# Performance work log

Measured on AMD Instinct MI355X. Metric: run time of the kernel, lower is better.

## Reference

```python
import jax, jax.numpy as jnp
import numpy as np
from jax import lax

B = 512
MBD_B, MBD_C = 64, 16
FEAT = 40 * 4 * 4  # 640


def _conv(x, w, b):
    y = lax.conv_general_dilated(x, w, (1, 1), 'VALID',
                                 dimension_numbers=('NCHW', 'OIHW', 'NCHW'))
    return y + b[None, :, None, None]


def _maxpool2(x):
    return lax.reduce_window(x, -jnp.inf, lax.max,
                             (1, 1, 2, 2), (1, 1, 2, 2), 'VALID')


def setup_inputs() -> dict:
    key = jax.random.key(0)
    ks = jax.random.split(key, 10)
    def he(k, shape, fan_in):
        return jax.random.normal(k, shape, dtype=jnp.float32) * np.float32(1.0 / np.sqrt(fan_in))
    return {
        'x': jax.random.normal(ks[0], (B, 1, 28, 28), dtype=jnp.float32),
        'conv1_w': he(ks[1], (20, 1, 5, 5), 25),
        'conv1_b': jnp.zeros((20,), jnp.float32),
        'conv2_w': he(ks[2], (40, 20, 5, 5), 20 * 25),
        'conv2_b': jnp.zeros((40,), jnp.float32),
        'T': he(ks[3], (MBD_B * MBD_C, FEAT), FEAT),          # feature_scan_tensor (no bias)
        'fc1_w': he(ks[4], (100, FEAT + MBD_B), FEAT + MBD_B),
        'fc1_b': jnp.zeros((100,), jnp.float32),
        'fc2_w': he(ks[5], (1, 100), 100),
        'fc2_b': jnp.zeros((1,), jnp.float32),
    }


def reference(x, conv1_w, conv1_b, conv2_w, conv2_b, T, fc1_w, fc1_b, fc2_w, fc2_b):
    # conv feature extractor: [B,1,28,28] -> [B,40,4,4]
    h = _maxpool2(jax.nn.relu(_conv(x, conv1_w, conv1_b)))
    h = _maxpool2(jax.nn.relu(_conv(h, conv2_w, conv2_b)))
    feats = h.reshape(h.shape[0], -1)  # [B, 640]

    # minibatch discrimination: M = feats @ T^T -> [B, b, c]
    M = (feats @ T.T).reshape(-1, MBD_B, MBD_C)
    # pairwise L1 over c: [B, B, b] (includes j==i diagonal = 0, exp(0)=1, as in original)
    dist = jnp.abs(M[:, None, :, :] - M[None, :, :, :]).sum(axis=3)
    closeness = jnp.exp(-dist).sum(axis=1)  # [B, b]

    out = jnp.concatenate([feats, closeness], axis=1)  # [B, 640+b]
    out = jax.nn.relu(out @ fc1_w.T + fc1_b)
    # Dropout(p=0.2) omitted (deterministic eval-mode reference)
    out = jax.nn.sigmoid(out @ fc2_w.T + fc2_b)  # [B, 1]
    return out
```

## Files before the change

### kernel.cpp

```cpp
#include <hip/hip_runtime.h>


#define NB 512

__global__ __launch_bounds__(256) void k1_conv1_pool(
    const float* __restrict__ x, const float* __restrict__ w,
    const float* __restrict__ bias, float* __restrict__ out) {
  __shared__ float img[784];
  __shared__ float wl[500];
  __shared__ float bl[20];
  const int imgId = blockIdx.x;
  {
    const float4* src = reinterpret_cast<const float4*>(x + imgId * 784);
    float4* dst = reinterpret_cast<float4*>(img);
    for (int t = threadIdx.x; t < 196; t += 256) dst[t] = src[t];
  }
  for (int t = threadIdx.x; t < 500; t += 256) wl[t] = w[t];
  if (threadIdx.x < 20) bl[threadIdx.x] = bias[threadIdx.x];
  __syncthreads();

  for (int o = threadIdx.x; o < 2880; o += 256) {
    const int ch = o / 144;
    const int rem = o - ch * 144;
    const int py = rem / 12;
    const int px = rem - py * 12;
    const int oy = py * 2, ox = px * 2;
    float p[6][6];
    const float* ib = &img[oy * 28 + ox];
#pragma unroll
    for (int r = 0; r < 6; ++r) {
      const float2 v0 = *reinterpret_cast<const float2*>(&ib[r * 28 + 0]);
      const float2 v1 = *reinterpret_cast<const float2*>(&ib[r * 28 + 2]);
      const float2 v2 = *reinterpret_cast<const float2*>(&ib[r * 28 + 4]);
      p[r][0] = v0.x; p[r][1] = v0.y; p[r][2] = v1.x;
      p[r][3] = v1.y; p[r][4] = v2.x; p[r][5] = v2.y;
    }
    const float* wc = &wl[ch * 25];
    float s00 = 0.f, s01 = 0.f, s10 = 0.f, s11 = 0.f;
#pragma unroll
    for (int ky = 0; ky < 5; ++ky) {
#pragma unroll
      for (int kx = 0; kx < 5; ++kx) {
        const float ww = wc[ky * 5 + kx];
        s00 += p[ky][kx] * ww;
        s01 += p[ky][kx + 1] * ww;
        s10 += p[ky + 1][kx] * ww;
        s11 += p[ky + 1][kx + 1] * ww;
      }
    }
    const float m = fmaxf(fmaxf(s00, s01), fmaxf(s10, s11)) + bl[ch];
    out[imgId * 2880 + o] = fmaxf(m, 0.f);
  }
}

__global__ __launch_bounds__(256) void k2_conv2_pool(
    const float* __restrict__ h1, const float* __restrict__ w,
    const float* __restrict__ bias, float* __restrict__ feats) {
  __shared__ float in[2880];
  __shared__ float wt[2][2][25][64];
  __shared__ float part[128][21];
  const int imgId = blockIdx.x;
  const int tid = threadIdx.x;
  const int h = tid >> 7;
  const int chg = (tid >> 4) & 7;
  const int pos = tid & 15;
  const int py = pos >> 2, px = pos & 3;
  const int oy = py * 2, ox = px * 2;

  {
    const float4* src = reinterpret_cast<const float4*>(h1 + imgId * 2880);
    float4* dst = reinterpret_cast<float4*>(in);
    for (int t = tid; t < 720; t += 256) dst[t] = src[t];
  }
  for (int e = tid; e < 2000; e += 256) {
    const int eh = (e >= 1000) ? 1 : 0;
    const int e2 = e - eh * 1000;
    const int oc = e2 / 25, tap = e2 - oc * 25;
    wt[eh][0][tap][(oc / 5) * 8 + (oc - (oc / 5) * 5)] =
        w[oc * 500 + (eh ? 10 : 0) * 25 + tap];
  }
  __syncthreads();

  float acc[5][4];
#pragma unroll
  for (int q = 0; q < 5; ++q)
#pragma unroll
    for (int pp = 0; pp < 4; ++pp) acc[q][pp] = 0.f;

  for (int s = 0; s < 10; ++s) {
    const int p0 = s & 1;
    float sv[8];
    if (s < 9) {
#pragma unroll
      for (int k = 0; k < 8; ++k) {
        const int e = tid + k * 256;
        if (e < 2000) {
          const int eh = (e >= 1000) ? 1 : 0;
          const int e2 = e - eh * 1000;
          const int oc = e2 / 25, tap = e2 - oc * 25;
          const int ic = eh ? (11 + s) : (s + 1);
          sv[k] = w[oc * 500 + ic * 25 + tap];
        }
      }
    }
    const int myic = h * 10 + s;
    float p[6][6];
    {
      const float* ib = &in[myic * 144 + oy * 12 + ox];
#pragma unroll
      for (int r = 0; r < 6; ++r) {
        const float2 v0 = *reinterpret_cast<const float2*>(&ib[r * 12 + 0]);
        const float2 v1 = *reinterpret_cast<const float2*>(&ib[r * 12 + 2]);
        const float2 v2 = *reinterpret_cast<const float2*>(&ib[r * 12 + 4]);
        p[r][0] = v0.x; p[r][1] = v0.y; p[r][2] = v1.x;
        p[r][3] = v1.y; p[r][4] = v2.x; p[r][5] = v2.y;
      }
    }
#pragma unroll
    for (int ky = 0; ky < 5; ++ky) {
#pragma unroll
      for (int kx = 0; kx < 5; ++kx) {
        const int tap = ky * 5 + kx;
        const float4 w4 =
            *reinterpret_cast<const float4*>(&wt[h][p0][tap][chg * 8]);
        const float w4b = wt[h][p0][tap][chg * 8 + 4];
        const float i00 = p[ky][kx];
        const float i01 = p[ky][kx + 1];
        const float i10 = p[ky + 1][kx];
        const float i11 = p[ky + 1][kx + 1];
        acc[0][0] += i00 * w4.x; acc[0][1] += i01 * w4.x;
        acc[0][2] += i10 * w4.x; acc[0][3] += i11 * w4.x;
        acc[1][0] += i00 * w4.y; acc[1][1] += i01 * w4.y;
        acc[1][2] += i10 * w4.y; acc[1][3] += i11 * w4.y;
        acc[2][0] += i00 * w4.z; acc[2][1] += i01 * w4.z;
        acc[2][2] += i10 * w4.z; acc[2][3] += i11 * w4.z;
        acc[3][0] += i00 * w4.w; acc[3][1] += i01 * w4.w;
        acc[3][2] += i10 * w4.w; acc[3][3] += i11 * w4.w;
        acc[4][0] += i00 * w4b; acc[4][1] += i01 * w4b;
        acc[4][2] += i10 * w4b; acc[4][3] += i11 * w4b;
      }
    }
    if (s < 9) {
#pragma unroll
      for (int k = 0; k < 8; ++k) {
        const int e = tid + k * 256;
        if (e < 2000) {
          const int eh = (e >= 1000) ? 1 : 0;
          const int e2 = e - eh * 1000;
          const int oc = e2 / 25, tap = e2 - oc * 25;
          wt[eh][(s + 1) & 1][tap][(oc / 5) * 8 + (oc - (oc / 5) * 5)] = sv[k];
        }
      }
    }
    __syncthreads();
  }

  if (tid >= 128) {
    const int t2 = tid - 128;
#pragma unroll
    for (int q = 0; q < 5; ++q)
#pragma unroll
      for (int pp = 0; pp < 4; ++pp) part[t2][q * 4 + pp] = acc[q][pp];
  }
  __syncthreads();
  if (tid < 128) {
#pragma unroll
    for (int q = 0; q < 5; ++q) {
      const int ch = chg * 5 + q;
      const float a0 = acc[q][0] + part[tid][q * 4 + 0];
      const float a1 = acc[q][1] + part[tid][q * 4 + 1];
      const float a2 = acc[q][2] + part[tid][q * 4 + 2];
      const float a3 = acc[q][3] + part[tid][q * 4 + 3];
      const float m = fmaxf(fmaxf(a0, a1), fmaxf(a2, a3)) + bias[ch];
      feats[imgId * 640 + ch * 16 + pos] = fmaxf(m, 0.f);
    }
  }
}

__global__ __launch_bounds__(256) void k3_gemm(
    const float* __restrict__ A, const float* __restrict__ Bm,
    float* __restrict__ C) {
  __shared__ float As[16][68];
  __shared__ float Bs[16][36];
  const int tid = threadIdx.x;
  const int tx = tid & 15;
  const int ty = tid >> 4;
  const int i0 = blockIdx.y * 64;
  const int j0 = blockIdx.x * 32;
  float acc[4][2];
#pragma unroll
  for (int u = 0; u < 4; ++u)
#pragma unroll
    for (int v = 0; v < 2; ++v) acc[u][v] = 0.f;

  for (int k0 = 0; k0 < 640; k0 += 16) {
    {
      const int m = tid >> 2, kq = tid & 3;
      const float4 av =
          *reinterpret_cast<const float4*>(A + (i0 + m) * 640 + k0 + kq * 4);
      As[kq * 4 + 0][m] = av.x;
      As[kq * 4 + 1][m] = av.y;
      As[kq * 4 + 2][m] = av.z;
      As[kq * 4 + 3][m] = av.w;
    }
    if (tid < 128) {
      const int n = tid >> 2, kq = tid & 3;
      const float4 bv =
          *reinterpret_cast<const float4*>(Bm + (j0 + n) * 640 + k0 + kq * 4);
      Bs[kq * 4 + 0][n] = bv.x;
      Bs[kq * 4 + 1][n] = bv.y;
      Bs[kq * 4 + 2][n] = bv.z;
      Bs[kq * 4 + 3][n] = bv.w;
    }
    __syncthreads();
#pragma unroll
    for (int kk = 0; kk < 16; ++kk) {
      const float4 a4 = *reinterpret_cast<const float4*>(&As[kk][ty * 4]);
      const float2 b2 = *reinterpret_cast<const float2*>(&Bs[kk][tx * 2]);
      acc[0][0] += a4.x * b2.x; acc[0][1] += a4.x * b2.y;
      acc[1][0] += a4.y * b2.x; acc[1][1] += a4.y * b2.y;
      acc[2][0] += a4.z * b2.x; acc[2][1] += a4.z * b2.y;
      acc[3][0] += a4.w * b2.x; acc[3][1] += a4.w * b2.y;
    }
    __syncthreads();
  }
#pragma unroll
  for (int u = 0; u < 4; ++u) {
    float2 st = make_float2(acc[u][0], acc[u][1]);
    *reinterpret_cast<float2*>(&C[(i0 + ty * 4 + u) * 1024 + j0 + tx * 2]) = st;
  }
}

__global__ __launch_bounds__(256) void k4_mbd(const float* __restrict__ M,
                                              float* __restrict__ cp) {
  const int bid = blockIdx.x;
  const int ig = bid >> 4;
  const int jq = bid & 15;
  const int t = threadIdx.x;
  const int b = t & 63;
  const int g = t >> 6;
  const int i0 = ig * 16 + g * 4;
  float4 mi[4][4];
#pragma unroll
  for (int u = 0; u < 4; ++u) {
    const float4* mp = reinterpret_cast<const float4*>(M + (i0 + u) * 1024 + b * 16);
    mi[u][0] = mp[0]; mi[u][1] = mp[1]; mi[u][2] = mp[2]; mi[u][3] = mp[3];
  }
  float acc[4] = {0.f, 0.f, 0.f, 0.f};
  for (int jj = 0; jj < 32; ++jj) {
    const int j = jq * 32 + jj;
    const float4* mjp = reinterpret_cast<const float4*>(M + j * 1024 + b * 16);
    const float4 mj0 = mjp[0], mj1 = mjp[1], mj2 = mjp[2], mj3 = mjp[3];
#pragma unroll
    for (int u = 0; u < 4; ++u) {
      float dist =
          fabsf(mi[u][0].x - mj0.x) + fabsf(mi[u][0].y - mj0.y) +
          fabsf(mi[u][0].z - mj0.z) + fabsf(mi[u][0].w - mj0.w) +
          fabsf(mi[u][1].x - mj1.x) + fabsf(mi[u][1].y - mj1.y) +
          fabsf(mi[u][1].z - mj1.z) + fabsf(mi[u][1].w - mj1.w) +
          fabsf(mi[u][2].x - mj2.x) + fabsf(mi[u][2].y - mj2.y) +
          fabsf(mi[u][2].z - mj2.z) + fabsf(mi[u][2].w - mj2.w) +
          fabsf(mi[u][3].x - mj3.x) + fabsf(mi[u][3].y - mj3.y) +
          fabsf(mi[u][3].z - mj3.z) + fabsf(mi[u][3].w - mj3.w);
      acc[u] += __expf(-dist);
    }
  }
#pragma unroll
  for (int u = 0; u < 4; ++u)
    cp[(jq * 512 + i0 + u) * 64 + b] = acc[u];
}

__global__ __launch_bounds__(128) void k5_head(
    const float* __restrict__ feats, const float* __restrict__ cp,
    const float* __restrict__ w1, const float* __restrict__ b1,
    const float* __restrict__ w2, const float* __restrict__ b2,
    float* __restrict__ out) {
  __shared__ float v[704];
  __shared__ float hb[100];
  const int i = blockIdx.x;
  for (int t = threadIdx.x; t < 640; t += 128) v[t] = feats[i * 640 + t];
  if (threadIdx.x < 64) {
    float s = 0.f;
#pragma unroll
    for (int q = 0; q < 16; ++q) s += cp[(q * 512 + i) * 64 + threadIdx.x];
    v[640 + threadIdx.x] = s;
  }
  __syncthreads();
  const int k = threadIdx.x;
  if (k < 100) {
    const float* wr = w1 + k * 704;
    float s = b1[k];
#pragma unroll 4
    for (int d = 0; d < 704; d += 4) {
      const float4 wv = *reinterpret_cast<const float4*>(wr + d);
      s += v[d] * wv.x + v[d + 1] * wv.y + v[d + 2] * wv.z + v[d + 3] * wv.w;
    }
    hb[k] = fmaxf(s, 0.f) * w2[k];
  }
  __syncthreads();
  if (threadIdx.x == 0) {
    float s = b2[0];
#pragma unroll 4
    for (int q = 0; q < 100; ++q) s += hb[q];
    out[i] = 1.f / (1.f + __expf(-s));
  }
}

extern "C" void kernel_launch(void* const* d_in, const int* in_sizes, int n_in,
                              void* d_out, int out_size, void* d_ws,
                              size_t ws_size, hipStream_t stream) {
  const float* x   = (const float*)d_in[0];
  const float* c1w = (const float*)d_in[1];
  const float* c1b = (const float*)d_in[2];
  const float* c2w = (const float*)d_in[3];
  const float* c2b = (const float*)d_in[4];
  const float* T   = (const float*)d_in[5];
  const float* f1w = (const float*)d_in[6];
  const float* f1b = (const float*)d_in[7];
  const float* f2w = (const float*)d_in[8];
  const float* f2b = (const float*)d_in[9];
  float* out = (float*)d_out;

  float* h1    = (float*)d_ws;
  float* feats = h1 + 512 * 2880;
  float* M     = feats + 512 * 640;
  float* cp    = h1;

  k1_conv1_pool<<<NB, 256, 0, stream>>>(x, c1w, c1b, h1);
  k2_conv2_pool<<<NB, 256, 0, stream>>>(h1, c2w, c2b, feats);
  k3_gemm<<<dim3(32, 8), 256, 0, stream>>>(feats, T, M);
  k4_mbd<<<NB, 256, 0, stream>>>(M, cp);
  k5_head<<<NB, 128, 0, stream>>>(feats, cp, f1w, f1b, f2w, f2b, out);
}
```

Measured before the change: 203.8 us.

## Split conv kernels per channel half, pre-transform conv2 weights, stage MBD rows in LDS

```diff
diff --git a/kernel.cpp b/kernel.cpp
--- a/kernel.cpp
+++ b/kernel.cpp
@@ -1,27 +1,43 @@
 #include <hip/hip_runtime.h>
 
 
-#define NB 512
-
-__global__ __launch_bounds__(256) void k1_conv1_pool(
+__global__ __launch_bounds__(256) void k0_wxform(const float* __restrict__ w,
+                                                 float* __restrict__ ws) {
+  const int e = blockIdx.x * 256 + threadIdx.x;
+  if (e >= 32000) return;
+  const int ocHalf = e / 16000;
+  const int r = e - ocHalf * 16000;
+  const int ic = r / 800;
+  const int r2 = r - ic * 800;
+  const int tap = r2 >> 5;
+  const int slot = r2 & 31;
+  const int q = slot & 7;
+  const int grp = slot >> 3;
+  float val = 0.f;
+  if (q < 5) val = w[(ocHalf * 20 + grp * 5 + q) * 500 + ic * 25 + tap];
+  ws[e] = val;
+}
+
+__global__ __launch_bounds__(128) void k1_conv1_pool(
     const float* __restrict__ x, const float* __restrict__ w,
     const float* __restrict__ bias, float* __restrict__ out) {
-  __shared__ float img[784];
-  __shared__ float wl[500];
-  __shared__ float bl[20];
-  const int imgId = blockIdx.x;
+  __shared__ __align__(16) float img[784];
+  __shared__ float wl[250];
+  __shared__ float bl[10];
+  const int imgId = blockIdx.x >> 1;
+  const int half = blockIdx.x & 1;
   {
     const float4* src = reinterpret_cast<const float4*>(x + imgId * 784);
     float4* dst = reinterpret_cast<float4*>(img);
-    for (int t = threadIdx.x; t < 196; t += 256) dst[t] = src[t];
-  }
-  for (int t = threadIdx.x; t < 500; t += 256) wl[t] = w[t];
-  if (threadIdx.x < 20) bl[threadIdx.x] = bias[threadIdx.x];
-  __syncthreads();
-
-  for (int o = threadIdx.x; o < 2880; o += 256) {
-    const int ch = o / 144;
-    const int rem = o - ch * 144;
+    for (int t = threadIdx.x; t < 196; t += 128) dst[t] = src[t];
+  }
+  for (int t = threadIdx.x; t < 250; t += 128) wl[t] = w[half * 250 + t];
+  if (threadIdx.x < 10) bl[threadIdx.x] = bias[half * 10 + threadIdx.x];
+  __syncthreads();
+
+  for (int o = threadIdx.x; o < 1440; o += 128) {
+    const int chl = o / 144;
+    const int rem = o - chl * 144;
     const int py = rem / 12;
     const int px = rem - py * 12;
     const int oy = py * 2, ox = px * 2;
@@ -35,7 +51,7 @@
       p[r][0] = v0.x; p[r][1] = v0.y; p[r][2] = v1.x;
       p[r][3] = v1.y; p[r][4] = v2.x; p[r][5] = v2.y;
     }
-    const float* wc = &wl[ch * 25];
+    const float* wc = &wl[chl * 25];
     float s00 = 0.f, s01 = 0.f, s10 = 0.f, s11 = 0.f;
 #pragma unroll
     for (int ky = 0; ky < 5; ++ky) {
@@ -48,21 +64,22 @@
         s11 += p[ky + 1][kx + 1] * ww;
       }
     }
-    const float m = fmaxf(fmaxf(s00, s01), fmaxf(s10, s11)) + bl[ch];
-    out[imgId * 2880 + o] = fmaxf(m, 0.f);
-  }
-}
-
-__global__ __launch_bounds__(256) void k2_conv2_pool(
-    const float* __restrict__ h1, const float* __restrict__ w,
+    const float m = fmaxf(fmaxf(s00, s01), fmaxf(s10, s11)) + bl[chl];
+    out[imgId * 2880 + half * 1440 + o] = fmaxf(m, 0.f);
+  }
+}
+
+__global__ __launch_bounds__(128) void k2_conv2_pool(
+    const float* __restrict__ h1, const float* __restrict__ wsx,
     const float* __restrict__ bias, float* __restrict__ feats) {
-  __shared__ float in[2880];
-  __shared__ float wt[2][2][25][64];
-  __shared__ float part[128][21];
-  const int imgId = blockIdx.x;
+  __shared__ __align__(16) float in[2880];
+  __shared__ __align__(16) float wl[2][2][25][32];
+  __shared__ float part[64][21];
+  const int imgId = blockIdx.x >> 1;
+  const int half = blockIdx.x & 1;
   const int tid = threadIdx.x;
-  const int h = tid >> 7;
-  const int chg = (tid >> 4) & 7;
+  const int h = tid >> 6;
+  const int grp = (tid >> 4) & 3;
   const int pos = tid & 15;
   const int py = pos >> 2, px = pos & 3;
   const int oy = py * 2, ox = px * 2;
@@ -70,14 +87,20 @@
   {
     const float4* src = reinterpret_cast<const float4*>(h1 + imgId * 2880);
     float4* dst = reinterpret_cast<float4*>(in);
-    for (int t = tid; t < 720; t += 256) dst[t] = src[t];
-  }
-  for (int e = tid; e < 2000; e += 256) {
-    const int eh = (e >= 1000) ? 1 : 0;
-    const int e2 = e - eh * 1000;
-    const int oc = e2 / 25, tap = e2 - oc * 25;
-    wt[eh][0][tap][(oc / 5) * 8 + (oc - (oc / 5) * 5)] =
-        w[oc * 500 + (eh ? 10 : 0) * 25 + tap];
+    for (int t = tid; t < 720; t += 128) dst[t] = src[t];
+  }
+  const float4* wsrc = reinterpret_cast<const float4*>(wsx) + half * 4000;
+  float4* wdst = reinterpret_cast<float4*>(wl);
+  {
+#pragma unroll
+    for (int k = 0; k < 4; ++k) {
+      const int e = tid + k * 128;
+      if (e < 400) {
+        const int hs = (e >= 200) ? 1 : 0;
+        const int idx = e - hs * 200;
+        wdst[hs * 400 + idx] = wsrc[(hs * 10 + 0) * 200 + idx];
+      }
+    }
   }
   __syncthreads();
 
@@ -89,17 +112,15 @@
 
   for (int s = 0; s < 10; ++s) {
     const int p0 = s & 1;
-    float sv[8];
+    float4 sv[4];
     if (s < 9) {
 #pragma unroll
-      for (int k = 0; k < 8; ++k) {
-        const int e = tid + k * 256;
-        if (e < 2000) {
-          const int eh = (e >= 1000) ? 1 : 0;
-          const int e2 = e - eh * 1000;
-          const int oc = e2 / 25, tap = e2 - oc * 25;
-          const int ic = eh ? (11 + s) : (s + 1);
-          sv[k] = w[oc * 500 + ic * 25 + tap];
+      for (int k = 0; k < 4; ++k) {
+        const int e = tid + k * 128;
+        if (e < 400) {
+          const int hs = (e >= 200) ? 1 : 0;
+          const int idx = e - hs * 200;
+          sv[k] = wsrc[(hs * 10 + s + 1) * 200 + idx];
         }
       }
     }
@@ -122,8 +143,8 @@
       for (int kx = 0; kx < 5; ++kx) {
         const int tap = ky * 5 + kx;
         const float4 w4 =
-            *reinterpret_cast<const float4*>(&wt[h][p0][tap][chg * 8]);
-        const float w4b = wt[h][p0][tap][chg * 8 + 4];
+            *reinterpret_cast<const float4*>(&wl[h][p0][tap][grp * 8]);
+        const float w4b = wl[h][p0][tap][grp * 8 + 4];
         const float i00 = p[ky][kx];
         const float i01 = p[ky][kx + 1];
         const float i10 = p[ky + 1][kx];
@@ -142,31 +163,30 @@
     }
     if (s < 9) {
 #pragma unroll
-      for (int k = 0; k < 8; ++k) {
-        const int e = tid + k * 256;
-        if (e < 2000) {
-          const int eh = (e >= 1000) ? 1 : 0;
-          const int e2 = e - eh * 1000;
-          const int oc = e2 / 25, tap = e2 - oc * 25;
-          wt[eh][(s + 1) & 1][tap][(oc / 5) * 8 + (oc - (oc / 5) * 5)] = sv[k];
+      for (int k = 0; k < 4; ++k) {
+        const int e = tid + k * 128;
+        if (e < 400) {
+          const int hs = (e >= 200) ? 1 : 0;
+          const int idx = e - hs * 200;
+          wdst[hs * 400 + ((s + 1) & 1) * 200 + idx] = sv[k];
         }
       }
     }
     __syncthreads();
   }
 
-  if (tid >= 128) {
-    const int t2 = tid - 128;
+  if (tid >= 64) {
+    const int t2 = tid - 64;
 #pragma unroll
     for (int q = 0; q < 5; ++q)
 #pragma unroll
       for (int pp = 0; pp < 4; ++pp) part[t2][q * 4 + pp] = acc[q][pp];
   }
   __syncthreads();
-  if (tid < 128) {
+  if (tid < 64) {
 #pragma unroll
     for (int q = 0; q < 5; ++q) {
-      const int ch = chg * 5 + q;
+      const int ch = half * 20 + grp * 5 + q;
       const float a0 = acc[q][0] + part[tid][q * 4 + 0];
       const float a1 = acc[q][1] + part[tid][q * 4 + 1];
       const float a2 = acc[q][2] + part[tid][q * 4 + 2];
@@ -177,24 +197,20 @@
   }
 }
 
-__global__ __launch_bounds__(256) void k3_gemm(
+__global__ __launch_bounds__(128) void k3_gemm(
     const float* __restrict__ A, const float* __restrict__ Bm,
     float* __restrict__ C) {
-  __shared__ float As[16][68];
-  __shared__ float Bs[16][36];
+  __shared__ __align__(16) float As[16][36];
+  __shared__ __align__(16) float Bs[16][36];
   const int tid = threadIdx.x;
   const int tx = tid & 15;
   const int ty = tid >> 4;
-  const int i0 = blockIdx.y * 64;
+  const int i0 = blockIdx.y * 16;
   const int j0 = blockIdx.x * 32;
-  float acc[4][2];
-#pragma unroll
-  for (int u = 0; u < 4; ++u)
-#pragma unroll
-    for (int v = 0; v < 2; ++v) acc[u][v] = 0.f;
+  float acc[2][2] = {{0.f, 0.f}, {0.f, 0.f}};
 
   for (int k0 = 0; k0 < 640; k0 += 16) {
-    {
+    if (tid < 64) {
       const int m = tid >> 2, kq = tid & 3;
       const float4 av =
           *reinterpret_cast<const float4*>(A + (i0 + m) * 640 + k0 + kq * 4);
@@ -203,7 +219,7 @@
       As[kq * 4 + 2][m] = av.z;
       As[kq * 4 + 3][m] = av.w;
     }
-    if (tid < 128) {
+    {
       const int n = tid >> 2, kq = tid & 3;
       const float4 bv =
           *reinterpret_cast<const float4*>(Bm + (j0 + n) * 640 + k0 + kq * 4);
@@ -215,24 +231,23 @@
     __syncthreads();
 #pragma unroll
     for (int kk = 0; kk < 16; ++kk) {
-      const float4 a4 = *reinterpret_cast<const float4*>(&As[kk][ty * 4]);
+      const float2 a2 = *reinterpret_cast<const float2*>(&As[kk][ty * 2]);
       const float2 b2 = *reinterpret_cast<const float2*>(&Bs[kk][tx * 2]);
-      acc[0][0] += a4.x * b2.x; acc[0][1] += a4.x * b2.y;
-      acc[1][0] += a4.y * b2.x; acc[1][1] += a4.y * b2.y;
-      acc[2][0] += a4.z * b2.x; acc[2][1] += a4.z * b2.y;
-      acc[3][0] += a4.w * b2.x; acc[3][1] += a4.w * b2.y;
+      acc[0][0] += a2.x * b2.x; acc[0][1] += a2.x * b2.y;
+      acc[1][0] += a2.y * b2.x; acc[1][1] += a2.y * b2.y;
     }
     __syncthreads();
   }
 #pragma unroll
-  for (int u = 0; u < 4; ++u) {
+  for (int u = 0; u < 2; ++u) {
     float2 st = make_float2(acc[u][0], acc[u][1]);
-    *reinterpret_cast<float2*>(&C[(i0 + ty * 4 + u) * 1024 + j0 + tx * 2]) = st;
+    *reinterpret_cast<float2*>(&C[(i0 + ty * 2 + u) * 1024 + j0 + tx * 2]) = st;
   }
 }
 
 __global__ __launch_bounds__(256) void k4_mbd(const float* __restrict__ M,
                                               float* __restrict__ cp) {
+  __shared__ float4 jb4[2][4][256];
   const int bid = blockIdx.x;
   const int ig = bid >> 4;
   const int jq = bid & 15;
@@ -240,69 +255,108 @@
   const int b = t & 63;
   const int g = t >> 6;
   const int i0 = ig * 16 + g * 4;
+  const float4* Mf4 = reinterpret_cast<const float4*>(M);
+
   float4 mi[4][4];
 #pragma unroll
   for (int u = 0; u < 4; ++u) {
-    const float4* mp = reinterpret_cast<const float4*>(M + (i0 + u) * 1024 + b * 16);
-    mi[u][0] = mp[0]; mi[u][1] = mp[1]; mi[u][2] = mp[2]; mi[u][3] = mp[3];
-  }
+#pragma unroll
+    for (int q = 0; q < 4; ++q) mi[u][q] = Mf4[(i0 + u) * 256 + b * 4 + q];
+  }
+  const int wslot = (t >> 2) * 4 + ((t & 3) ^ ((t >> 3) & 3));
+  {
+#pragma unroll
+    for (int k = 0; k < 4; ++k)
+      jb4[0][k][wslot] = Mf4[(jq * 32 + k) * 256 + t];
+  }
+  __syncthreads();
+
   float acc[4] = {0.f, 0.f, 0.f, 0.f};
-  for (int jj = 0; jj < 32; ++jj) {
-    const int j = jq * 32 + jj;
-    const float4* mjp = reinterpret_cast<const float4*>(M + j * 1024 + b * 16);
-    const float4 mj0 = mjp[0], mj1 = mjp[1], mj2 = mjp[2], mj3 = mjp[3];
-#pragma unroll
-    for (int u = 0; u < 4; ++u) {
-      float dist =
-          fabsf(mi[u][0].x - mj0.x) + fabsf(mi[u][0].y - mj0.y) +
-          fabsf(mi[u][0].z - mj0.z) + fabsf(mi[u][0].w - mj0.w) +
-          fabsf(mi[u][1].x - mj1.x) + fabsf(mi[u][1].y - mj1.y) +
-          fabsf(mi[u][1].z - mj1.z) + fabsf(mi[u][1].w - mj1.w) +
-          fabsf(mi[u][2].x - mj2.x) + fabsf(mi[u][2].y - mj2.y) +
-          fabsf(mi[u][2].z - mj2.z) + fabsf(mi[u][2].w - mj2.w) +
-          fabsf(mi[u][3].x - mj3.x) + fabsf(mi[u][3].y - mj3.y) +
-          fabsf(mi[u][3].z - mj3.z) + fabsf(mi[u][3].w - mj3.w);
-      acc[u] += __expf(-dist);
-    }
+  const int xr = (b >> 1) & 3;
+  for (int c = 0; c < 8; ++c) {
+    float4 st[4];
+    if (c < 7) {
+#pragma unroll
+      for (int k = 0; k < 4; ++k)
+        st[k] = Mf4[(jq * 32 + (c + 1) * 4 + k) * 256 + t];
+    }
+    const int cbuf = c & 1;
+#pragma unroll
+    for (int jj = 0; jj < 4; ++jj) {
+      const float4* row = jb4[cbuf][jj];
+      float4 mj[4];
+#pragma unroll
+      for (int q = 0; q < 4; ++q) mj[q] = row[b * 4 + (q ^ xr)];
+#pragma unroll
+      for (int u = 0; u < 4; ++u) {
+        float dist =
+            fabsf(mi[u][0].x - mj[0].x) + fabsf(mi[u][0].y - mj[0].y) +
+            fabsf(mi[u][0].z - mj[0].z) + fabsf(mi[u][0].w - mj[0].w) +
+            fabsf(mi[u][1].x - mj[1].x) + fabsf(mi[u][1].y - mj[1].y) +
+            fabsf(mi[u][1].z - mj[1].z) + fabsf(mi[u][1].w - mj[1].w) +
+            fabsf(mi[u][2].x - mj[2].x) + fabsf(mi[u][2].y - mj[2].y) +
+            fabsf(mi[u][2].z - mj[2].z) + fabsf(mi[u][2].w - mj[2].w) +
+            fabsf(mi[u][3].x - mj[3].x) + fabsf(mi[u][3].y - mj[3].y) +
+            fabsf(mi[u][3].z - mj[3].z) + fabsf(mi[u][3].w - mj[3].w);
+        acc[u] += __expf(-dist);
+      }
+    }
+    if (c < 7) {
+#pragma unroll
+      for (int k = 0; k < 4; ++k) jb4[(c + 1) & 1][k][wslot] = st[k];
+    }
+    __syncthreads();
   }
 #pragma unroll
   for (int u = 0; u < 4; ++u)
     cp[(jq * 512 + i0 + u) * 64 + b] = acc[u];
 }
 
-__global__ __launch_bounds__(128) void k5_head(
+__global__ __launch_bounds__(256) void k5_head(
     const float* __restrict__ feats, const float* __restrict__ cp,
     const float* __restrict__ w1, const float* __restrict__ b1,
     const float* __restrict__ w2, const float* __restrict__ b2,
     float* __restrict__ out) {
-  __shared__ float v[704];
+  __shared__ __align__(16) float v[704];
   __shared__ float hb[100];
   const int i = blockIdx.x;
-  for (int t = threadIdx.x; t < 640; t += 128) v[t] = feats[i * 640 + t];
-  if (threadIdx.x < 64) {
+  const int tid = threadIdx.x;
+  float4* v4 = reinterpret_cast<float4*>(v);
+  if (tid < 160)
+    v4[tid] = reinterpret_cast<const float4*>(feats + i * 640)[tid];
+  if (tid >= 192) {
+    const int bb = tid - 192;
     float s = 0.f;
 #pragma unroll
-    for (int q = 0; q < 16; ++q) s += cp[(q * 512 + i) * 64 + threadIdx.x];
-    v[640 + threadIdx.x] = s;
-  }
-  __syncthreads();
-  const int k = threadIdx.x;
-  if (k < 100) {
-    const float* wr = w1 + k * 704;
-    float s = b1[k];
-#pragma unroll 4
-    for (int d = 0; d < 704; d += 4) {
-      const float4 wv = *reinterpret_cast<const float4*>(wr + d);
-      s += v[d] * wv.x + v[d + 1] * wv.y + v[d + 2] * wv.z + v[d + 3] * wv.w;
-    }
-    hb[k] = fmaxf(s, 0.f) * w2[k];
-  }
-  __syncthreads();
-  if (threadIdx.x == 0) {
-    float s = b2[0];
-#pragma unroll 4
-    for (int q = 0; q < 100; ++q) s += hb[q];
-    out[i] = 1.f / (1.f + __expf(-s));
+    for (int q = 0; q < 16; ++q) s += cp[(q * 512 + i) * 64 + bb];
+    v[640 + bb] = s;
+  }
+  __syncthreads();
+  const int wave = tid >> 6;
+  const int lane = tid & 63;
+  for (int r = wave; r < 100; r += 4) {
+    const float4* wr = reinterpret_cast<const float4*>(w1 + r * 704);
+    const float4 wa = wr[lane];
+    const float4 wb = wr[lane + 64];
+    const float4 va = v4[lane];
+    const float4 vb = v4[lane + 64];
+    float s = wa.x * va.x + wa.y * va.y + wa.z * va.z + wa.w * va.w +
+              wb.x * vb.x + wb.y * vb.y + wb.z * vb.z + wb.w * vb.w;
+    if (lane < 48) {
+      const float4 wc = wr[lane + 128];
+      const float4 vc = v4[lane + 128];
+      s += wc.x * vc.x + wc.y * vc.y + wc.z * vc.z + wc.w * vc.w;
+    }
+#pragma unroll
+    for (int off = 32; off; off >>= 1) s += __shfl_xor(s, off);
+    if (lane == 0) hb[r] = fmaxf(s + b1[r], 0.f) * w2[r];
+  }
+  __syncthreads();
+  if (tid < 64) {
+    float s = hb[tid] + ((tid < 36) ? hb[tid + 64] : 0.f);
+#pragma unroll
+    for (int off = 32; off; off >>= 1) s += __shfl_xor(s, off);
+    if (tid == 0) out[i] = 1.f / (1.f + __expf(-(s + b2[0])));
   }
 }
 
@@ -321,14 +375,16 @@
   const float* f2b = (const float*)d_in[9];
   float* out = (float*)d_out;
 
-  float* h1    = (float*)d_ws;
-  float* feats = h1 + 512 * 2880;
-  float* M     = feats + 512 * 640;
-  float* cp    = h1;
-
-  k1_conv1_pool<<<NB, 256, 0, stream>>>(x, c1w, c1b, h1);
-  k2_conv2_pool<<<NB, 256, 0, stream>>>(h1, c2w, c2b, feats);
-  k3_gemm<<<dim3(32, 8), 256, 0, stream>>>(feats, T, M);
-  k4_mbd<<<NB, 256, 0, stream>>>(M, cp);
-  k5_head<<<NB, 128, 0, stream>>>(feats, cp, f1w, f1b, f2w, f2b, out);
-}
+  float* h1     = (float*)d_ws;
+  float* feats  = h1 + 512 * 2880;
+  float* M      = feats + 512 * 640;
+  float* wstage = M;
+  float* cp     = h1;
+
+  k0_wxform<<<125, 256, 0, stream>>>(c2w, wstage);
+  k1_conv1_pool<<<1024, 128, 0, stream>>>(x, c1w, c1b, h1);
+  k2_conv2_pool<<<1024, 128, 0, stream>>>(h1, wstage, c2b, feats);
+  k3_gemm<<<dim3(32, 32), 128, 0, stream>>>(feats, T, M);
+  k4_mbd<<<512, 256, 0, stream>>>(M, cp);
+  k5_head<<<512, 256, 0, stream>>>(feats, cp, f1w, f1b, f2w, f2b, out);
+}
```

After: 195.4 us. 1.04x faster.
